# Optimization experiments

Measured on AMD Instinct MI355X. Metric: run time of the kernel, lower is better.

## Reference

```python
import jax, jax.numpy as jnp
import numpy as np

B, S, D = 8, 2048, 512

def setup_inputs() -> dict:
    key = jax.random.key(0)
    k1, k2, k3, k4, k5 = jax.random.split(key, 5)
    scale_w = 1.0 / np.sqrt(D)
    return {
        "input_vector": jax.random.normal(k1, (B, S, D), dtype=jnp.float32),
        "mask": jax.random.randint(k2, (B, S), 0, 2, dtype=jnp.int32),
        "Wq": jax.random.normal(k3, (D, D), dtype=jnp.float32) * scale_w,
        "Wk": jax.random.normal(k4, (D, D), dtype=jnp.float32) * scale_w,
        "Wv": jax.random.normal(k5, (D, D), dtype=jnp.float32) * scale_w,
    }

def reference(input_vector, mask, Wq, Wk, Wv):
    # torch nn.Linear(bias=False): x @ W.T
    q = jnp.einsum('bsd,ed->bse', input_vector, Wq)
    k = jnp.einsum('bsd,ed->bse', input_vector, Wk)
    v = jnp.einsum('bsd,ed->bse', input_vector, Wv)
    # NOTE: original scales by sqrt(k.size(1)) == sqrt(seq_len), a quirk we preserve.
    scale = jnp.asarray(S, q.dtype) ** 0.5
    scores = jnp.einsum('bqd,bkd->bqk', q, k) / scale  # [B,S,S]
    m = mask[:, None, :]  # unsqueeze(1) -> broadcast over query dim
    scores = jnp.where(m == 0, -jnp.inf, scores)
    probs = jax.nn.softmax(scores, axis=-1)
    return jnp.einsum('bqk,bkd->bqd', probs, v)
```

## Files before the change

kernel.cpp:

```cpp
#include <hip/hip_runtime.h>
#include <cstdint>
#include <cstddef>

#define BB 8
#define SS 2048
#define DD 512

typedef __attribute__((ext_vector_type(8))) short bf16x8;
typedef __attribute__((ext_vector_type(4))) float f32x4;

__device__ __forceinline__ unsigned short f2bf(float f) {
  unsigned int u = __builtin_bit_cast(unsigned int, f);
  u = (u + 0x7FFFu + ((u >> 16) & 1u)) >> 16;
  return (unsigned short)u;
}
__device__ __forceinline__ float bf2f(unsigned short s) {
  return __builtin_bit_cast(float, ((unsigned int)s) << 16);
}

__device__ __forceinline__ void gload_lds16(const unsigned short* g, unsigned short* l) {
  __builtin_amdgcn_global_load_lds(
      (const __attribute__((address_space(1))) void*)g,
      (__attribute__((address_space(3))) void*)l, 16, 0, 0);
}

__device__ __forceinline__ void gemm_tile(
    const unsigned short* __restrict__ A,
    const unsigned short* __restrict__ B,
    int K, unsigned short* lA, unsigned short* lB,
    f32x4 acc[4][4], size_t m0, size_t n0)
{
  const int t = threadIdx.x;
  const int l = t & 63;
  const int w = t >> 6;
  const int wr = w >> 1, wc = w & 1;
  const size_t K64 = (size_t)K * 64;

  const unsigned short* gA = A + (m0 + (size_t)(t >> 2)) * (size_t)K + (size_t)((t & 3) * 8);
  const unsigned short* gB = B + (n0 + (size_t)(t >> 2)) * (size_t)K + (size_t)((t & 3) * 8);

  const int ar = (wr * 64 + (l & 15)) * 32 + (l >> 4) * 8;
  const int br = (wc * 64 + (l & 15)) * 32 + (l >> 4) * 8;

  const int nk = K >> 5;
  int buf = 0;

  gload_lds16(gA, lA + t * 8);
  gload_lds16(gA + K64, lA + 2048 + t * 8);
  gload_lds16(gB, lB + t * 8);
  gload_lds16(gB + K64, lB + 2048 + t * 8);

  for (int kt = 0; kt < nk; ++kt) {
    __syncthreads();
    if (kt + 1 < nk) {
      const int ko = (kt + 1) << 5;
      const int lo = (buf ^ 1) * 4096;
      gload_lds16(gA + ko, lA + lo + t * 8);
      gload_lds16(gA + ko + K64, lA + lo + 2048 + t * 8);
      gload_lds16(gB + ko, lB + lo + t * 8);
      gload_lds16(gB + ko + K64, lB + lo + 2048 + t * 8);
    }
    const unsigned short* pa = lA + buf * 4096 + ar;
    const unsigned short* pb = lB + buf * 4096 + br;
    bf16x8 af[4], bfr[4];
#pragma unroll
    for (int m = 0; m < 4; ++m) af[m] = *(const bf16x8*)(pa + m * 512);
#pragma unroll
    for (int n = 0; n < 4; ++n) bfr[n] = *(const bf16x8*)(pb + n * 512);
#pragma unroll
    for (int m = 0; m < 4; ++m)
#pragma unroll
      for (int n = 0; n < 4; ++n)
        acc[m][n] = __builtin_amdgcn_mfma_f32_16x16x32_bf16(af[m], bfr[n], acc[m][n], 0, 0, 0);
    buf ^= 1;
  }
}

__global__ __launch_bounds__(256) void convert_k(
    const float* __restrict__ X, const float* __restrict__ Wq,
    const float* __restrict__ Wk, const float* __restrict__ Wv,
    unsigned short* __restrict__ dst)
{
  const size_t NXe = (size_t)BB * SS * DD;
  const size_t NWe = (size_t)DD * DD;
  size_t i = ((size_t)blockIdx.x * 256 + threadIdx.x) * 4;
  const float* src;
  size_t off;
  if (i < NXe)                { src = X;  off = i; }
  else if (i < NXe + NWe)     { src = Wq; off = i - NXe; }
  else if (i < NXe + 2 * NWe) { src = Wk; off = i - NXe - NWe; }
  else                        { src = Wv; off = i - NXe - 2 * NWe; }
  float4 f = *(const float4*)(src + off);
  ushort4 o;
  o.x = f2bf(f.x); o.y = f2bf(f.y); o.z = f2bf(f.z); o.w = f2bf(f.w);
  *(ushort4*)(dst + i) = o;
}

__global__ __launch_bounds__(256, 2) void qkv_gemm_k(
    const unsigned short* __restrict__ Xb,
    const unsigned short* __restrict__ Wall,
    unsigned short* __restrict__ Qb,
    unsigned short* __restrict__ Kb,
    unsigned short* __restrict__ Vtb)
{
  __shared__ __align__(16) unsigned short lA[8192];
  __shared__ __align__(16) unsigned short lB[8192];
  const int z = blockIdx.z;
  const unsigned short* Bw = Wall + (size_t)z * (DD * DD);
  const size_t m0 = (size_t)blockIdx.y * 128;
  const size_t n0 = (size_t)blockIdx.x * 128;
  f32x4 acc[4][4];
#pragma unroll
  for (int m = 0; m < 4; ++m)
#pragma unroll
    for (int n = 0; n < 4; ++n) acc[m][n] = (f32x4){0.f, 0.f, 0.f, 0.f};

  gemm_tile(Xb, Bw, DD, lA, lB, acc, m0, n0);

  const int t = threadIdx.x, l = t & 63, w = t >> 6, wr = w >> 1, wc = w & 1;
  const size_t rb = m0 + (size_t)(wr * 64 + ((l >> 4) * 4));
  const int cb = (int)n0 + wc * 64 + (l & 15);
  if (z < 2) {
    unsigned short* O = z ? Kb : Qb;
#pragma unroll
    for (int m = 0; m < 4; ++m)
#pragma unroll
      for (int n = 0; n < 4; ++n)
#pragma unroll
        for (int j = 0; j < 4; ++j) {
          size_t r = rb + (size_t)(m * 16 + j);
          O[r * DD + (size_t)(cb + n * 16)] = f2bf(acc[m][n][j]);
        }
  } else {
#pragma unroll
    for (int m = 0; m < 4; ++m)
#pragma unroll
      for (int n = 0; n < 4; ++n)
#pragma unroll
        for (int j = 0; j < 4; ++j) {
          size_t r = rb + (size_t)(m * 16 + j);
          size_t bb = r >> 11, s = r & 2047;
          Vtb[((bb * DD + (size_t)(cb + n * 16)) << 11) + s] = f2bf(acc[m][n][j]);
        }
  }
}

__global__ __launch_bounds__(256, 2) void scores_gemm_k(
    const unsigned short* __restrict__ Qb,
    const unsigned short* __restrict__ Kb,
    unsigned short* __restrict__ Sc)
{
  __shared__ __align__(16) unsigned short lA[8192];
  __shared__ __align__(16) unsigned short lB[8192];
  const int b = blockIdx.z;
  const unsigned short* A  = Qb + (size_t)b * (SS * DD);
  const unsigned short* Bp = Kb + (size_t)b * (SS * DD);
  unsigned short* C = Sc + (size_t)b * ((size_t)SS * SS);
  const size_t m0 = (size_t)blockIdx.y * 128;
  const size_t n0 = (size_t)blockIdx.x * 128;
  f32x4 acc[4][4];
#pragma unroll
  for (int m = 0; m < 4; ++m)
#pragma unroll
    for (int n = 0; n < 4; ++n) acc[m][n] = (f32x4){0.f, 0.f, 0.f, 0.f};

  gemm_tile(A, Bp, DD, lA, lB, acc, m0, n0);

  const int t = threadIdx.x, l = t & 63, w = t >> 6, wr = w >> 1, wc = w & 1;
  const size_t rb = m0 + (size_t)(wr * 64 + ((l >> 4) * 4));
  const int cb = (int)n0 + wc * 64 + (l & 15);
#pragma unroll
  for (int m = 0; m < 4; ++m)
#pragma unroll
    for (int n = 0; n < 4; ++n)
#pragma unroll
      for (int j = 0; j < 4; ++j) {
        size_t r = rb + (size_t)(m * 16 + j);
        C[r * SS + (size_t)(cb + n * 16)] = f2bf(acc[m][n][j]);
      }
}

__global__ __launch_bounds__(256) void softmax_k(
    unsigned short* __restrict__ Sc, const int* __restrict__ mask)
{
  __shared__ float smax[4], ssum[4];
  const int row = blockIdx.x;
  const int b = row >> 11;
  unsigned short* p = Sc + (size_t)row * SS;
  const int* mk = mask + ((size_t)b << 11);
  const int t = threadIdx.x;
  const int c0 = t * 8;

  bf16x8 sv = *(const bf16x8*)(p + c0);
  int4 ma = *(const int4*)(mk + c0);
  int4 mb = *(const int4*)(mk + c0 + 4);
  int mm[8] = {ma.x, ma.y, ma.z, ma.w, mb.x, mb.y, mb.z, mb.w};
  const float SCALE = 0.022097086912079608f;
  float v[8];
#pragma unroll
  for (int j = 0; j < 8; ++j) v[j] = bf2f((unsigned short)sv[j]) * SCALE;

  float mx = -3.0e38f;
#pragma unroll
  for (int j = 0; j < 8; ++j) if (mm[j]) mx = fmaxf(mx, v[j]);
#pragma unroll
  for (int off = 32; off >= 1; off >>= 1) mx = fmaxf(mx, __shfl_xor(mx, off));
  const int wid = t >> 6, ln = t & 63;
  if (ln == 0) smax[wid] = mx;
  __syncthreads();
  mx = fmaxf(fmaxf(smax[0], smax[1]), fmaxf(smax[2], smax[3]));

  float e[8];
  float sum = 0.f;
#pragma unroll
  for (int j = 0; j < 8; ++j) { e[j] = mm[j] ? __expf(v[j] - mx) : 0.f; sum += e[j]; }
#pragma unroll
  for (int off = 32; off >= 1; off >>= 1) sum += __shfl_xor(sum, off);
  if (ln == 0) ssum[wid] = sum;
  __syncthreads();
  sum = ssum[0] + ssum[1] + ssum[2] + ssum[3];
  const float inv = 1.f / sum;

  bf16x8 ov;
#pragma unroll
  for (int j = 0; j < 8; ++j) ov[j] = (short)f2bf(e[j] * inv);
  *(bf16x8*)(p + c0) = ov;
}

__global__ __launch_bounds__(256, 2) void pv_gemm_k(
    const unsigned short* __restrict__ Sc,
    const unsigned short* __restrict__ Vtb,
    float* __restrict__ Out)
{
  __shared__ __align__(16) unsigned short lA[8192];
  __shared__ __align__(16) unsigned short lB[8192];
  const int b = blockIdx.z;
  const unsigned short* A  = Sc + (size_t)b * ((size_t)SS * SS);
  const unsigned short* Bp = Vtb + (size_t)b * (DD * SS);
  float* C = Out + (size_t)b * (SS * DD);
  const size_t m0 = (size_t)blockIdx.y * 128;
  const size_t n0 = (size_t)blockIdx.x * 128;
  f32x4 acc[4][4];
#pragma unroll
  for (int m = 0; m < 4; ++m)
#pragma unroll
    for (int n = 0; n < 4; ++n) acc[m][n] = (f32x4){0.f, 0.f, 0.f, 0.f};

  gemm_tile(A, Bp, SS, lA, lB, acc, m0, n0);

  const int t = threadIdx.x, l = t & 63, w = t >> 6, wr = w >> 1, wc = w & 1;
  const size_t rb = m0 + (size_t)(wr * 64 + ((l >> 4) * 4));
  const int cb = (int)n0 + wc * 64 + (l & 15);
#pragma unroll
  for (int m = 0; m < 4; ++m)
#pragma unroll
    for (int n = 0; n < 4; ++n)
#pragma unroll
      for (int j = 0; j < 4; ++j) {
        size_t r = rb + (size_t)(m * 16 + j);
        C[r * DD + (size_t)(cb + n * 16)] = acc[m][n][j];
      }
}

extern "C" void kernel_launch(void* const* d_in, const int* in_sizes, int n_in,
                              void* d_out, int out_size, void* d_ws, size_t ws_size,
                              hipStream_t stream) {
  const float* X    = (const float*)d_in[0];
  const int*   mask = (const int*)d_in[1];
  const float* Wq   = (const float*)d_in[2];
  const float* Wk   = (const float*)d_in[3];
  const float* Wv   = (const float*)d_in[4];

  unsigned short* ws  = (unsigned short*)d_ws;
  unsigned short* Xb   = ws;
  unsigned short* Wall = ws + 8388608;
  unsigned short* Qb   = ws + 9175040;
  unsigned short* Kb   = ws + 17563648;
  unsigned short* Vtb  = ws + 25952256;
  unsigned short* Sc   = ws + 34340864;
  float* Out = (float*)d_out;

  convert_k<<<8960, 256, 0, stream>>>(X, Wq, Wk, Wv, ws);

  qkv_gemm_k<<<dim3(4, 128, 3), 256, 0, stream>>>(Xb, Wall, Qb, Kb, Vtb);

  scores_gemm_k<<<dim3(16, 16, 8), 256, 0, stream>>>(Qb, Kb, Sc);

  softmax_k<<<16384, 256, 0, stream>>>(Sc, mask);

  pv_gemm_k<<<dim3(4, 16, 8), 256, 0, stream>>>(Sc, Vtb, Out);
}
```

Before: 276.8 us.

## Fuse scores, softmax and PV into a single flash-attention kernel

Replaces the separate scores GEMM, softmax and PV GEMM kernels with one kernel using an online softmax. Each block handles 64 queries and streams K and transposed-V tiles through double-buffered LDS using global_load_lds with XOR swizzles. Probabilities are staged per wave through a small LDS buffer for the PV MFMA. This removes the write and re-read of the full B×S×S bf16 score matrix. The cost is one block per CU with only 4 waves, heavy register use (32 output accumulators plus Q fragments) and a serialized per-tile softmax with many lane shuffles, which may leave it latency-bound.

```diff
diff --git a/kernel.cpp b/kernel.cpp
--- a/kernel.cpp
+++ b/kernel.cpp
@@ -145,121 +145,165 @@
   }
 }
 
-__global__ __launch_bounds__(256, 2) void scores_gemm_k(
+__device__ __forceinline__ void stage_K(const unsigned short* __restrict__ Kg,
+                                        int kt, unsigned short* dst, int t) {
+#pragma unroll
+  for (int p = 0; p < 8; ++p) {
+    int row = 4 * p + (t >> 6);
+    int lslot = (t & 63) ^ (row & 7);
+    gload_lds16(Kg + (size_t)(kt * 32 + row) * DD + lslot * 8,
+                dst + p * 2048 + t * 8);
+  }
+}
+
+__device__ __forceinline__ void stage_V(const unsigned short* __restrict__ Vg,
+                                        int kt, unsigned short* dst, int t) {
+#pragma unroll
+  for (int p = 0; p < 8; ++p) {
+    int d = 64 * p + (t >> 2);
+    int lslot = (t & 3) ^ ((d >> 1) & 3);
+    gload_lds16(Vg + (size_t)d * SS + kt * 32 + lslot * 8,
+                dst + p * 2048 + t * 8);
+  }
+}
+
+__global__ __launch_bounds__(256, 1) void fused_attn_k(
     const unsigned short* __restrict__ Qb,
     const unsigned short* __restrict__ Kb,
-    unsigned short* __restrict__ Sc)
-{
-  __shared__ __align__(16) unsigned short lA[8192];
-  __shared__ __align__(16) unsigned short lB[8192];
-  const int b = blockIdx.z;
-  const unsigned short* A  = Qb + (size_t)b * (SS * DD);
-  const unsigned short* Bp = Kb + (size_t)b * (SS * DD);
-  unsigned short* C = Sc + (size_t)b * ((size_t)SS * SS);
-  const size_t m0 = (size_t)blockIdx.y * 128;
-  const size_t n0 = (size_t)blockIdx.x * 128;
-  f32x4 acc[4][4];
-#pragma unroll
-  for (int m = 0; m < 4; ++m)
-#pragma unroll
-    for (int n = 0; n < 4; ++n) acc[m][n] = (f32x4){0.f, 0.f, 0.f, 0.f};
-
-  gemm_tile(A, Bp, DD, lA, lB, acc, m0, n0);
-
-  const int t = threadIdx.x, l = t & 63, w = t >> 6, wr = w >> 1, wc = w & 1;
-  const size_t rb = m0 + (size_t)(wr * 64 + ((l >> 4) * 4));
-  const int cb = (int)n0 + wc * 64 + (l & 15);
-#pragma unroll
-  for (int m = 0; m < 4; ++m)
-#pragma unroll
-    for (int n = 0; n < 4; ++n)
-#pragma unroll
-      for (int j = 0; j < 4; ++j) {
-        size_t r = rb + (size_t)(m * 16 + j);
-        C[r * SS + (size_t)(cb + n * 16)] = f2bf(acc[m][n][j]);
-      }
-}
-
-__global__ __launch_bounds__(256) void softmax_k(
-    unsigned short* __restrict__ Sc, const int* __restrict__ mask)
-{
-  __shared__ float smax[4], ssum[4];
-  const int row = blockIdx.x;
-  const int b = row >> 11;
-  unsigned short* p = Sc + (size_t)row * SS;
-  const int* mk = mask + ((size_t)b << 11);
-  const int t = threadIdx.x;
-  const int c0 = t * 8;
-
-  bf16x8 sv = *(const bf16x8*)(p + c0);
-  int4 ma = *(const int4*)(mk + c0);
-  int4 mb = *(const int4*)(mk + c0 + 4);
-  int mm[8] = {ma.x, ma.y, ma.z, ma.w, mb.x, mb.y, mb.z, mb.w};
-  const float SCALE = 0.022097086912079608f;
-  float v[8];
-#pragma unroll
-  for (int j = 0; j < 8; ++j) v[j] = bf2f((unsigned short)sv[j]) * SCALE;
-
-  float mx = -3.0e38f;
-#pragma unroll
-  for (int j = 0; j < 8; ++j) if (mm[j]) mx = fmaxf(mx, v[j]);
-#pragma unroll
-  for (int off = 32; off >= 1; off >>= 1) mx = fmaxf(mx, __shfl_xor(mx, off));
-  const int wid = t >> 6, ln = t & 63;
-  if (ln == 0) smax[wid] = mx;
-  __syncthreads();
-  mx = fmaxf(fmaxf(smax[0], smax[1]), fmaxf(smax[2], smax[3]));
-
-  float e[8];
-  float sum = 0.f;
-#pragma unroll
-  for (int j = 0; j < 8; ++j) { e[j] = mm[j] ? __expf(v[j] - mx) : 0.f; sum += e[j]; }
-#pragma unroll
-  for (int off = 32; off >= 1; off >>= 1) sum += __shfl_xor(sum, off);
-  if (ln == 0) ssum[wid] = sum;
-  __syncthreads();
-  sum = ssum[0] + ssum[1] + ssum[2] + ssum[3];
-  const float inv = 1.f / sum;
-
-  bf16x8 ov;
-#pragma unroll
-  for (int j = 0; j < 8; ++j) ov[j] = (short)f2bf(e[j] * inv);
-  *(bf16x8*)(p + c0) = ov;
-}
-
-__global__ __launch_bounds__(256, 2) void pv_gemm_k(
-    const unsigned short* __restrict__ Sc,
     const unsigned short* __restrict__ Vtb,
+    const int* __restrict__ mask,
     float* __restrict__ Out)
 {
-  __shared__ __align__(16) unsigned short lA[8192];
-  __shared__ __align__(16) unsigned short lB[8192];
-  const int b = blockIdx.z;
-  const unsigned short* A  = Sc + (size_t)b * ((size_t)SS * SS);
-  const unsigned short* Bp = Vtb + (size_t)b * (DD * SS);
-  float* C = Out + (size_t)b * (SS * DD);
-  const size_t m0 = (size_t)blockIdx.y * 128;
-  const size_t n0 = (size_t)blockIdx.x * 128;
-  f32x4 acc[4][4];
-#pragma unroll
-  for (int m = 0; m < 4; ++m)
-#pragma unroll
-    for (int n = 0; n < 4; ++n) acc[m][n] = (f32x4){0.f, 0.f, 0.f, 0.f};
-
-  gemm_tile(A, Bp, SS, lA, lB, acc, m0, n0);
-
-  const int t = threadIdx.x, l = t & 63, w = t >> 6, wr = w >> 1, wc = w & 1;
-  const size_t rb = m0 + (size_t)(wr * 64 + ((l >> 4) * 4));
-  const int cb = (int)n0 + wc * 64 + (l & 15);
-#pragma unroll
-  for (int m = 0; m < 4; ++m)
-#pragma unroll
-    for (int n = 0; n < 4; ++n)
-#pragma unroll
-      for (int j = 0; j < 4; ++j) {
-        size_t r = rb + (size_t)(m * 16 + j);
-        C[r * DD + (size_t)(cb + n * 16)] = acc[m][n][j];
+  __shared__ __align__(16) unsigned short Kl[2][32 * 512];
+  __shared__ __align__(16) unsigned short Vl[2][512 * 32];
+  __shared__ __align__(16) unsigned short Pl[4][16 * 32];
+
+  const int t = threadIdx.x;
+  const int l = t & 63;
+  const int w = t >> 6;
+  const int b = blockIdx.y;
+  const size_t bs0 = (size_t)b * SS + (size_t)blockIdx.x * 64;
+
+  const unsigned short* Qg = Qb + (bs0 + (size_t)(w * 16)) * DD;
+  const unsigned short* Kg = Kb + (size_t)b * ((size_t)SS * DD);
+  const unsigned short* Vg = Vtb + (size_t)b * ((size_t)DD * SS);
+  const int* mk = mask + ((size_t)b << 11);
+
+  bf16x8 qf[16];
+  {
+    const unsigned short* qrow = Qg + (size_t)(l & 15) * DD + (l >> 4) * 8;
+#pragma unroll
+    for (int ks = 0; ks < 16; ++ks) qf[ks] = *(const bf16x8*)(qrow + ks * 32);
+  }
+
+  f32x4 oacc[32];
+#pragma unroll
+  for (int fn = 0; fn < 32; ++fn) oacc[fn] = (f32x4){0.f, 0.f, 0.f, 0.f};
+  float mrow[4] = {-1e30f, -1e30f, -1e30f, -1e30f};
+  float lrow[4] = {0.f, 0.f, 0.f, 0.f};
+
+  const float SCALE = 0.022097086912079608f;
+
+  stage_K(Kg, 0, Kl[0], t);
+  stage_V(Vg, 0, Vl[0], t);
+
+  int buf = 0;
+  for (int kt = 0; kt < 64; ++kt) {
+    __syncthreads();
+    if (kt + 1 < 64) {
+      stage_K(Kg, kt + 1, Kl[buf ^ 1], t);
+      stage_V(Vg, kt + 1, Vl[buf ^ 1], t);
+    }
+
+    f32x4 sacc[2];
+    sacc[0] = (f32x4){0.f, 0.f, 0.f, 0.f};
+    sacc[1] = (f32x4){0.f, 0.f, 0.f, 0.f};
+    const unsigned short* Kc = Kl[buf];
+#pragma unroll
+    for (int fn = 0; fn < 2; ++fn) {
+      const int key = fn * 16 + (l & 15);
+      const unsigned short* krow = Kc + key * 512;
+      const int kx = key & 7;
+#pragma unroll
+      for (int ks = 0; ks < 16; ++ks) {
+        int slot = ks * 4 + (l >> 4);
+        bf16x8 kf = *(const bf16x8*)(krow + ((slot ^ kx) * 8));
+        sacc[fn] = __builtin_amdgcn_mfma_f32_16x16x32_bf16(qf[ks], kf, sacc[fn], 0, 0, 0);
       }
+    }
+
+    const int mk0 = mk[kt * 32 + (l & 15)];
+    const int mk1 = mk[kt * 32 + 16 + (l & 15)];
+    float scl[4];
+    unsigned short p0[4], p1[4];
+#pragma unroll
+    for (int j = 0; j < 4; ++j) {
+      float s0 = mk0 ? sacc[0][j] * SCALE : -1e30f;
+      float s1 = mk1 ? sacc[1][j] * SCALE : -1e30f;
+      float mx = fmaxf(s0, s1);
+      mx = fmaxf(mx, __shfl_xor(mx, 1));
+      mx = fmaxf(mx, __shfl_xor(mx, 2));
+      mx = fmaxf(mx, __shfl_xor(mx, 4));
+      mx = fmaxf(mx, __shfl_xor(mx, 8));
+      float mnew = fmaxf(mrow[j], mx);
+      scl[j] = __expf(mrow[j] - mnew);
+      mrow[j] = mnew;
+      float e0 = mk0 ? __expf(s0 - mnew) : 0.f;
+      float e1 = mk1 ? __expf(s1 - mnew) : 0.f;
+      float r = e0 + e1;
+      r += __shfl_xor(r, 1);
+      r += __shfl_xor(r, 2);
+      r += __shfl_xor(r, 4);
+      r += __shfl_xor(r, 8);
+      lrow[j] = lrow[j] * scl[j] + r;
+      p0[j] = f2bf(e0);
+      p1[j] = f2bf(e1);
+    }
+
+#pragma unroll
+    for (int fn = 0; fn < 32; ++fn)
+#pragma unroll
+      for (int j = 0; j < 4; ++j) oacc[fn][j] *= scl[j];
+
+    unsigned short* Pw = Pl[w];
+#pragma unroll
+    for (int j = 0; j < 4; ++j) {
+      int row = (l >> 4) * 4 + j;
+      int x = ((row >> 1) & 3) << 3;
+      Pw[row * 32 + (((l & 15)) ^ x)]      = p0[j];
+      Pw[row * 32 + ((16 + (l & 15)) ^ x)] = p1[j];
+    }
+    bf16x8 pf;
+    {
+      int row = l & 15;
+      int slot = (l >> 4) ^ ((row >> 1) & 3);
+      pf = *(const bf16x8*)(Pw + row * 32 + slot * 8);
+    }
+
+    const unsigned short* Vc = Vl[buf];
+#pragma unroll
+    for (int fn = 0; fn < 32; ++fn) {
+      int d = fn * 16 + (l & 15);
+      int slot = (l >> 4) ^ ((d >> 1) & 3);
+      bf16x8 vf = *(const bf16x8*)(Vc + d * 32 + slot * 8);
+      oacc[fn] = __builtin_amdgcn_mfma_f32_16x16x32_bf16(pf, vf, oacc[fn], 0, 0, 0);
+    }
+    buf ^= 1;
+  }
+
+  float inv[4];
+#pragma unroll
+  for (int j = 0; j < 4; ++j) inv[j] = 1.f / lrow[j];
+  float* Og = Out + (bs0 + (size_t)(w * 16)) * DD;
+#pragma unroll
+  for (int fn = 0; fn < 32; ++fn) {
+    int d = fn * 16 + (l & 15);
+#pragma unroll
+    for (int j = 0; j < 4; ++j) {
+      int row = (l >> 4) * 4 + j;
+      Og[(size_t)row * DD + d] = oacc[fn][j] * inv[j];
+    }
+  }
 }
 
 extern "C" void kernel_launch(void* const* d_in, const int* in_sizes, int n_in,
@@ -271,22 +315,17 @@
   const float* Wk   = (const float*)d_in[3];
   const float* Wv   = (const float*)d_in[4];
 
-  unsigned short* ws  = (unsigned short*)d_ws;
+  unsigned short* ws   = (unsigned short*)d_ws;
   unsigned short* Xb   = ws;
   unsigned short* Wall = ws + 8388608;
   unsigned short* Qb   = ws + 9175040;
   unsigned short* Kb   = ws + 17563648;
   unsigned short* Vtb  = ws + 25952256;
-  unsigned short* Sc   = ws + 34340864;
   float* Out = (float*)d_out;
 
   convert_k<<<8960, 256, 0, stream>>>(X, Wq, Wk, Wv, ws);
 
   qkv_gemm_k<<<dim3(4, 128, 3), 256, 0, stream>>>(Xb, Wall, Qb, Kb, Vtb);
 
-  scores_gemm_k<<<dim3(16, 16, 8), 256, 0, stream>>>(Qb, Kb, Sc);
-
-  softmax_k<<<16384, 256, 0, stream>>>(Sc, mask);
-
-  pv_gemm_k<<<dim3(4, 16, 8), 256, 0, stream>>>(Sc, Vtb, Out);
-}
+  fused_attn_k<<<dim3(32, 8), 256, 0, stream>>>(Qb, Kb, Vtb, mask, Out);
+}
```

After: 358.2 us. 29.4% more time.
